# Optimization experiments

Measured on AMD Instinct MI355X. Metric: run time of the kernel, lower is better.

The kernel has to match this reference:

```python
import jax, jax.numpy as jnp
import numpy as np

N_DIMS = 16  # n points per block; nAngs = n*(n-1)/2 = 120


def orthmtx(angles, n):
    """Batched Givens-rotation cascade: angles (B, n(n-1)/2) -> (B, n, n) orthonormal."""
    nb = angles.shape[0]
    M = jnp.broadcast_to(jnp.eye(n, dtype=angles.dtype), (nb, n, n))
    k = 0
    for iTop in range(n - 1):
        vt = M[:, iTop, :]  # (B, n)
        for iBtm in range(iTop + 1, n):
            a = angles[:, k]
            c = jnp.cos(a)[:, None]
            s = jnp.sin(a)[:, None]
            vb = M[:, iBtm, :]
            vt, vb = c * vt - s * vb, s * vt + c * vb
            M = M.at[:, iBtm, :].set(vb)
            k += 1
        M = M.at[:, iTop, :].set(vt)
    return M


def setup_inputs() -> dict:
    key = jax.random.key(0)
    k1, k2 = jax.random.split(key)
    nblks, n, m = 1024, N_DIMS, 2048
    nangs = n * (n - 1) // 2
    X = jax.random.normal(k1, (nblks, n, m), dtype=jnp.float32)
    angles = jax.random.normal(k2, (nblks, nangs), dtype=jnp.float32)
    mus = jnp.ones((nblks, n), dtype=jnp.float32)
    return {"X": X, "angles": angles, "mus": mus}


def reference(X, angles, mus):
    n = X.shape[1]
    R = orthmtx(angles, n)                # (B, n, n)
    R = mus[:, :, None] * R              # sign flips per row
    return jnp.matmul(R, X)              # Analysis mode: R @ X -> (B, n, m)
```

## Files before the change

### kernel.cpp

```cpp
#include <hip/hip_runtime.h>

#define NDIM   16
#define MCOLS  2048
#define NANG   120
#define BLOCK  256
#define COLS_PER_WG 1024

typedef float f32x4 __attribute__((ext_vector_type(4)));

__global__ __launch_bounds__(BLOCK) void soot_kernel(
    const float* __restrict__ X,
    const float* __restrict__ angles,
    const float* __restrict__ mus,
    float* __restrict__ out)
{
    __shared__ float c_lds[NANG];
    __shared__ float s_lds[NANG];
    __shared__ __align__(16) float R_lds[NDIM * NDIM];

    const int wg   = blockIdx.x;
    const int b    = wg >> 1;
    const int half = wg & 1;
    const int tid  = threadIdx.x;

    const int col = half * COLS_PER_WG + tid * 4;
    const float* Xb = X   + (size_t)b * NDIM * MCOLS;
    float*       Ob = out + (size_t)b * NDIM * MCOLS;

    f32x4 x4[NDIM];
#pragma unroll
    for (int jj = 0; jj < NDIM; ++jj)
        x4[jj] = *reinterpret_cast<const f32x4*>(Xb + jj * MCOLS + col);

    if (tid < 64) {
#pragma unroll
        for (int rep = 0; rep < 2; ++rep) {
            const int k = tid + rep * 64;
            if (k < NANG) {
                float a = angles[b * NANG + k];
                float sv, cv;
                sincosf(a, &sv, &cv);
                c_lds[k] = cv;
                s_lds[k] = sv;
            }
        }
    }
    __syncthreads();

    if (tid < NDIM) {
        const int j = tid;
        float m[NDIM];
#pragma unroll
        for (int r = 0; r < NDIM; ++r) m[r] = (r == j) ? 1.0f : 0.0f;
        int k = 0;
#pragma unroll
        for (int iTop = 0; iTop < NDIM - 1; ++iTop) {
            float vt = m[iTop];
#pragma unroll
            for (int iBtm = iTop + 1; iBtm < NDIM; ++iBtm) {
                const float c  = c_lds[k];
                const float s  = s_lds[k];
                const float vb = m[iBtm];
                const float nvt = c * vt - s * vb;
                m[iBtm] = s * vt + c * vb;
                vt = nvt;
                ++k;
            }
            m[iTop] = vt;
        }
#pragma unroll
        for (int r = 0; r < NDIM; ++r)
            R_lds[r * NDIM + j] = mus[b * NDIM + r] * m[r];
    }
    __syncthreads();

#pragma unroll
    for (int r = 0; r < NDIM; ++r) {
        f32x4 acc = (f32x4)(0.f);
#pragma unroll
        for (int q = 0; q < 4; ++q) {
            const f32x4 w = *reinterpret_cast<const f32x4*>(&R_lds[r * NDIM + q * 4]);
#pragma unroll
            for (int t = 0; t < 4; ++t) {
                const float wv = w[t];
                acc += wv * x4[q * 4 + t];
            }
        }
        __builtin_nontemporal_store(acc, reinterpret_cast<f32x4*>(Ob + r * MCOLS + col));
    }
}

extern "C" void kernel_launch(void* const* d_in, const int* in_sizes, int n_in,
                              void* d_out, int out_size, void* d_ws, size_t ws_size,
                              hipStream_t stream) {
    const float* X      = (const float*)d_in[0];
    const float* angles = (const float*)d_in[1];
    const float* mus    = (const float*)d_in[2];
    float* out          = (float*)d_out;

    const int nblks = in_sizes[1] / NANG;
    dim3 grid(nblks * (MCOLS / COLS_PER_WG));
    dim3 block(BLOCK);
    hipLaunchKernelGGL(soot_kernel, grid, block, 0, stream,
                       X, angles, mus, out);
}
```

Before: 47.93 us.

## Split rotation-matrix build into separate kernel and apply via workspace

Moves the Givens-cascade construction of R into its own small kernel that writes R to a workspace buffer. A second kernel then loads R into LDS and streams X through it, with each workgroup covering both column halves of a block. The aim is to keep the serial sincos and cascade work from stalling the memory-bound matmul workgroups. The cost is a second launch, an extra global round trip for R, and half as many workgroups in the apply kernel. The fused kernel is kept as a fallback when the workspace is too small, and there it now loads X only after R is built.

```diff
diff --git a/kernel.cpp b/kernel.cpp
--- a/kernel.cpp
+++ b/kernel.cpp
@@ -8,7 +8,92 @@
 
 typedef float f32x4 __attribute__((ext_vector_type(4)));
 
-__global__ __launch_bounds__(BLOCK) void soot_kernel(
+__global__ __launch_bounds__(64) void build_R_kernel(
+    const float* __restrict__ angles,
+    const float* __restrict__ mus,
+    float* __restrict__ Rws)
+{
+    const int b    = blockIdx.x;
+    const int lane = threadIdx.x;
+    __shared__ float c_lds[NANG];
+    __shared__ float s_lds[NANG];
+
+#pragma unroll
+    for (int rep = 0; rep < 2; ++rep) {
+        const int k = lane + rep * 64;
+        if (k < NANG) {
+            float sv, cv;
+            sincosf(angles[b * NANG + k], &sv, &cv);
+            c_lds[k] = cv;
+            s_lds[k] = sv;
+        }
+    }
+    __syncthreads();
+
+    if (lane < NDIM) {
+        const int j = lane;
+        float m[NDIM];
+#pragma unroll
+        for (int r = 0; r < NDIM; ++r) m[r] = (r == j) ? 1.0f : 0.0f;
+        int k = 0;
+#pragma unroll
+        for (int iTop = 0; iTop < NDIM - 1; ++iTop) {
+            float vt = m[iTop];
+#pragma unroll
+            for (int iBtm = iTop + 1; iBtm < NDIM; ++iBtm) {
+                const float c  = c_lds[k];
+                const float s  = s_lds[k];
+                const float vb = m[iBtm];
+                const float nvt = c * vt - s * vb;
+                m[iBtm] = s * vt + c * vb;
+                vt = nvt;
+                ++k;
+            }
+            m[iTop] = vt;
+        }
+#pragma unroll
+        for (int r = 0; r < NDIM; ++r)
+            Rws[b * (NDIM * NDIM) + r * NDIM + j] = mus[b * NDIM + r] * m[r];
+    }
+}
+
+__global__ __launch_bounds__(BLOCK) void apply_kernel(
+    const float* __restrict__ X,
+    const float* __restrict__ Rws,
+    float* __restrict__ out)
+{
+    const int b   = blockIdx.x;
+    const int tid = threadIdx.x;
+    __shared__ __align__(16) float R_lds[NDIM * NDIM];
+
+    if (tid < 64)
+        *reinterpret_cast<f32x4*>(&R_lds[tid * 4]) =
+            *reinterpret_cast<const f32x4*>(&Rws[b * (NDIM * NDIM) + tid * 4]);
+    __syncthreads();
+
+    const float* Xb = X   + (size_t)b * NDIM * MCOLS;
+    float*       Ob = out + (size_t)b * NDIM * MCOLS;
+
+#pragma unroll
+    for (int chunk = 0; chunk < 2; ++chunk) {
+        const int col = chunk * COLS_PER_WG + tid * 4;
+        f32x4 x4[NDIM];
+#pragma unroll
+        for (int jj = 0; jj < NDIM; ++jj)
+            x4[jj] = *reinterpret_cast<const f32x4*>(Xb + jj * MCOLS + col);
+
+#pragma unroll
+        for (int r = 0; r < NDIM; ++r) {
+            f32x4 acc = (f32x4)(0.f);
+#pragma unroll
+            for (int q = 0; q < NDIM; ++q)
+                acc += R_lds[r * NDIM + q] * x4[q];
+            __builtin_nontemporal_store(acc, reinterpret_cast<f32x4*>(Ob + r * MCOLS + col));
+        }
+    }
+}
+
+__global__ __launch_bounds__(BLOCK) void soot_fused_kernel(
     const float* __restrict__ X,
     const float* __restrict__ angles,
     const float* __restrict__ mus,
@@ -22,15 +107,6 @@
     const int b    = wg >> 1;
     const int half = wg & 1;
     const int tid  = threadIdx.x;
-
-    const int col = half * COLS_PER_WG + tid * 4;
-    const float* Xb = X   + (size_t)b * NDIM * MCOLS;
-    float*       Ob = out + (size_t)b * NDIM * MCOLS;
-
-    f32x4 x4[NDIM];
-#pragma unroll
-    for (int jj = 0; jj < NDIM; ++jj)
-        x4[jj] = *reinterpret_cast<const f32x4*>(Xb + jj * MCOLS + col);
 
     if (tid < 64) {
 #pragma unroll
@@ -74,18 +150,21 @@
     }
     __syncthreads();
 
+    const int col = half * COLS_PER_WG + tid * 4;
+    const float* Xb = X   + (size_t)b * NDIM * MCOLS;
+    float*       Ob = out + (size_t)b * NDIM * MCOLS;
+
+    f32x4 x4[NDIM];
+#pragma unroll
+    for (int jj = 0; jj < NDIM; ++jj)
+        x4[jj] = *reinterpret_cast<const f32x4*>(Xb + jj * MCOLS + col);
+
 #pragma unroll
     for (int r = 0; r < NDIM; ++r) {
         f32x4 acc = (f32x4)(0.f);
 #pragma unroll
-        for (int q = 0; q < 4; ++q) {
-            const f32x4 w = *reinterpret_cast<const f32x4*>(&R_lds[r * NDIM + q * 4]);
-#pragma unroll
-            for (int t = 0; t < 4; ++t) {
-                const float wv = w[t];
-                acc += wv * x4[q * 4 + t];
-            }
-        }
+        for (int q = 0; q < NDIM; ++q)
+            acc += R_lds[r * NDIM + q] * x4[q];
         __builtin_nontemporal_store(acc, reinterpret_cast<f32x4*>(Ob + r * MCOLS + col));
     }
 }
@@ -99,8 +178,17 @@
     float* out          = (float*)d_out;
 
     const int nblks = in_sizes[1] / NANG;
-    dim3 grid(nblks * (MCOLS / COLS_PER_WG));
-    dim3 block(BLOCK);
-    hipLaunchKernelGGL(soot_kernel, grid, block, 0, stream,
-                       X, angles, mus, out);
+    const size_t ws_needed = (size_t)nblks * NDIM * NDIM * sizeof(float);
+
+    if (ws_size >= ws_needed) {
+        float* Rws = (float*)d_ws;
+        hipLaunchKernelGGL(build_R_kernel, dim3(nblks), dim3(64), 0, stream,
+                           angles, mus, Rws);
+        hipLaunchKernelGGL(apply_kernel, dim3(nblks), dim3(BLOCK), 0, stream,
+                           X, Rws, out);
+    } else {
+        hipLaunchKernelGGL(soot_fused_kernel,
+                           dim3(nblks * (MCOLS / COLS_PER_WG)), dim3(BLOCK), 0, stream,
+                           X, angles, mus, out);
+    }
 }
```

Result: slower. 59.93 us (+25.0%).
